# Kernel tuning notes

Measured on AMD Instinct MI355X. Metric: run time of the kernel, lower is better.

## Reference

```python
import jax, jax.numpy as jnp
import numpy as np

N = 50000   # nodes
E = 800000  # edges (avg degree 16)
D = 64      # feature dim (input_dim == hidden_dim == output_dim for num_layer=2)
BN_EPS = 1e-5


def setup_inputs() -> dict:
    key = jax.random.key(0)
    ks = jax.random.split(key, 8)
    def lin_w(k, fan_in, fan_out):
        return jax.random.normal(k, (fan_in, fan_out), jnp.float32) / np.sqrt(fan_in).astype(np.float32)
    inp = {
        "x": jax.random.normal(ks[0], (N, D), jnp.float32),
        "edge_index": jax.random.randint(ks[1], (2, E), 0, N),
    }
    ki = 2
    for l in range(2):
        for s in ("a", "b"):
            inp[f"w{l}{s}"] = lin_w(ks[ki], D, D)
            inp[f"b{l}{s}"] = jnp.zeros((D,), jnp.float32)
            inp[f"g{l}{s}"] = jnp.ones((D,), jnp.float32)   # BN gamma
            inp[f"be{l}{s}"] = jnp.zeros((D,), jnp.float32)  # BN beta
            ki += 1
    inp["lin_w"] = lin_w(ks[6], 2 * D, D)  # JK cat of 2 layers -> 2D, final lin -> D
    inp["lin_b"] = jnp.zeros((D,), jnp.float32)
    return inp


def _bn(h, g, b):
    # BatchNorm1d in training mode: batch statistics over the node axis
    m = h.mean(axis=0)
    v = h.var(axis=0)
    return (h - m) * jax.lax.rsqrt(v + BN_EPS) * g + b


def _gin(h, src, dst, w1, b1, g1, be1, w2, b2, g2, be2):
    # GINConv with eps=0: (1+eps)*x_i + sum_{j->i} x_j, then MLP(Lin-BN-ReLU-Lin-BN-ReLU)
    agg = jax.ops.segment_sum(h[src], dst, num_segments=N) + h
    h = jax.nn.relu(_bn(agg @ w1 + b1, g1, be1))
    return jax.nn.relu(_bn(h @ w2 + b2, g2, be2))


def reference(x, edge_index, w0a, b0a, g0a, be0a, w0b, b0b, g0b, be0b,
              w1a, b1a, g1a, be1a, w1b, b1b, g1b, be1b, lin_w, lin_b):
    src, dst = edge_index[0], edge_index[1]
    h1 = _gin(x, src, dst, w0a, b0a, g0a, be0a, w0b, b0b, g0b, be0b)
    h2 = _gin(h1, src, dst, w1a, b1a, g1a, be1a, w1b, b1b, g1b, be1b)
    # JumpingKnowledge 'cat' over the conv outputs (res[1:]), then final linear
    return jnp.concatenate([h1, h2], axis=1) @ lin_w + lin_b
```

## Files before the change

kernel.cpp:

```cpp
#include <hip/hip_runtime.h>
#include <hip/hip_bf16.h>

#define NN 50000
#define NE 800000
#define BN_EPS 1e-5f
#define CHUNK 8192
#define NCH 98
#define NBK 196

typedef __attribute__((ext_vector_type(4))) float f32x4;

__global__ void zero_k(int* __restrict__ p, int n) {
    int i = blockIdx.x * 256 + threadIdx.x;
    if (i < n) p[i] = 0;
}

__global__ void bhist_k(const int* __restrict__ dst, int* __restrict__ bcnt) {
    __shared__ int c[256];
    int t = threadIdx.x;
    c[t] = 0;
    __syncthreads();
    int base = blockIdx.x * CHUNK;
    int n = NE - base; if (n > CHUNK) n = CHUNK;
    for (int i = t; i < n; i += 256) atomicAdd(&c[dst[base + i] >> 8], 1);
    __syncthreads();
    if (c[t]) atomicAdd(&bcnt[t], c[t]);
}

__global__ void bscan_k(const int* __restrict__ bcnt, int* __restrict__ bbase,
                        int* __restrict__ bres, int* __restrict__ off) {
    __shared__ int s[256];
    int t = threadIdx.x;
    int v = bcnt[t];
    s[t] = v;
    __syncthreads();
    for (int d = 1; d < 256; d <<= 1) {
        int u = (t >= d) ? s[t - d] : 0;
        __syncthreads();
        s[t] += u;
        __syncthreads();
    }
    int ex = s[t] - v;
    bbase[t] = ex;
    bres[t] = ex;
    if (t == 0) { bbase[256] = NE; off[NN] = NE; }
}

__global__ void bscatter_k(const int* __restrict__ src, const int* __restrict__ dst,
                           int* __restrict__ bres, int* __restrict__ ebuf) {
    __shared__ int cnt[256], loff[256], lcur[256], gst[256], sc[256];
    __shared__ int packed[CHUNK];
    int t = threadIdx.x;
    cnt[t] = 0;
    __syncthreads();
    int base = blockIdx.x * CHUNK;
    int n = NE - base; if (n > CHUNK) n = CHUNK;
    for (int i = t; i < n; i += 256) atomicAdd(&cnt[dst[base + i] >> 8], 1);
    __syncthreads();
    sc[t] = cnt[t];
    __syncthreads();
    for (int d = 1; d < 256; d <<= 1) {
        int u = (t >= d) ? sc[t - d] : 0;
        __syncthreads();
        sc[t] += u;
        __syncthreads();
    }
    loff[t] = sc[t] - cnt[t];
    lcur[t] = loff[t];
    __syncthreads();
    for (int i = t; i < n; i += 256) {
        int d = dst[base + i];
        int b = d >> 8;
        int p = atomicAdd(&lcur[b], 1);
        packed[p] = src[base + i] | ((d & 255) << 16) | (b << 24);
    }
    __syncthreads();
    if (cnt[t]) gst[t] = atomicAdd(&bres[t], cnt[t]);
    __syncthreads();
    for (int i = t; i < n; i += 256) {
        int v = packed[i];
        int b = (v >> 24) & 255;
        ebuf[gst[b] + i - loff[b]] = v & 0xFFFFFF;
    }
}

__global__ void csr_k(const int* __restrict__ bbase, const int* __restrict__ ebuf,
                      int* __restrict__ off, int* __restrict__ adj) {
    __shared__ int cnt[256], loff[256], lcur[256], sc[256];
    int b = blockIdx.x, t = threadIdx.x;
    int s0 = bbase[b], s1 = bbase[b + 1];
    int n = s1 - s0;
    cnt[t] = 0;
    __syncthreads();
    for (int i = t; i < n; i += 256) atomicAdd(&cnt[(ebuf[s0 + i] >> 16) & 255], 1);
    __syncthreads();
    sc[t] = cnt[t];
    __syncthreads();
    for (int d = 1; d < 256; d <<= 1) {
        int u = (t >= d) ? sc[t - d] : 0;
        __syncthreads();
        sc[t] += u;
        __syncthreads();
    }
    loff[t] = sc[t] - cnt[t];
    lcur[t] = loff[t];
    int node = b * 256 + t;
    if (node < NN) off[node] = s0 + loff[t];
    __syncthreads();
    for (int i = t; i < n; i += 256) {
        int v = ebuf[s0 + i];
        int p = atomicAdd(&lcur[(v >> 16) & 255], 1);
        adj[s0 + p] = v & 0xFFFF;
    }
}

__device__ __forceinline__ float gather_row(const float* __restrict__ X, int ldx,
                                            int lane, const int* __restrict__ off,
                                            const int* __restrict__ adj, int node) {
    float acc = X[(size_t)node * ldx + lane];
    int s = off[node], e = off[node + 1];
    int p = s;
    for (; p + 8 <= e; p += 8) {
        int j0 = adj[p + 0], j1 = adj[p + 1], j2 = adj[p + 2], j3 = adj[p + 3];
        int j4 = adj[p + 4], j5 = adj[p + 5], j6 = adj[p + 6], j7 = adj[p + 7];
        float v0 = X[(size_t)j0 * ldx + lane];
        float v1 = X[(size_t)j1 * ldx + lane];
        float v2 = X[(size_t)j2 * ldx + lane];
        float v3 = X[(size_t)j3 * ldx + lane];
        float v4 = X[(size_t)j4 * ldx + lane];
        float v5 = X[(size_t)j5 * ldx + lane];
        float v6 = X[(size_t)j6 * ldx + lane];
        float v7 = X[(size_t)j7 * ldx + lane];
        acc += ((v0 + v1) + (v2 + v3)) + ((v4 + v5) + (v6 + v7));
    }
    if (p + 4 <= e) {
        int j0 = adj[p + 0], j1 = adj[p + 1], j2 = adj[p + 2], j3 = adj[p + 3];
        float v0 = X[(size_t)j0 * ldx + lane];
        float v1 = X[(size_t)j1 * ldx + lane];
        float v2 = X[(size_t)j2 * ldx + lane];
        float v3 = X[(size_t)j3 * ldx + lane];
        acc += (v0 + v1) + (v2 + v3);
        p += 4;
    }
    for (; p < e; p++) acc += X[(size_t)adj[p] * ldx + lane];
    return acc;
}

__global__ void ggemm_k(const float* __restrict__ X, int ldx,
                        const int* __restrict__ off, const int* __restrict__ adj,
                        const float* __restrict__ W,
                        const float* __restrict__ bias,
                        float* __restrict__ T,
                        float* __restrict__ sums) {
    __shared__ float As[64 * 65];
    __shared__ float Ws[64 * 64];
    __shared__ float lsum[64], lssq[64];
    int tid = threadIdx.x;
    int rowbase = blockIdx.x * 64;
    int wv = tid >> 6, lane = tid & 63;

    for (int i = tid; i < 1024; i += 256) {
        *(f32x4*)(Ws + i * 4) = *(const f32x4*)(W + i * 4);
    }
    if (tid < 64) { lsum[tid] = 0.f; lssq[tid] = 0.f; }

    for (int rr = 0; rr < 16; rr++) {
        int r = wv * 16 + rr;
        int node = rowbase + r;
        if (node >= NN) node = NN - 1;
        As[lane * 65 + r] = gather_row(X, ldx, lane, off, adj, node);
    }
    __syncthreads();

    int ty = tid >> 4, tx = tid & 15;
    float acc[4][4] = {};
    for (int k = 0; k < 64; k++) {
        float a[4], wvv[4];
        #pragma unroll
        for (int i = 0; i < 4; i++) a[i] = As[k * 65 + ty * 4 + i];
        #pragma unroll
        for (int j = 0; j < 4; j++) wvv[j] = Ws[k * 64 + tx * 4 + j];
        #pragma unroll
        for (int i = 0; i < 4; i++)
            #pragma unroll
            for (int j = 0; j < 4; j++) acc[i][j] += a[i] * wvv[j];
    }

    f32x4 bv = *(const f32x4*)(bias + tx * 4);
    float ps[4] = {0.f, 0.f, 0.f, 0.f}, pq[4] = {0.f, 0.f, 0.f, 0.f};
    #pragma unroll
    for (int i = 0; i < 4; i++) {
        int row = rowbase + ty * 4 + i;
        if (row < NN) {
            f32x4 v;
            #pragma unroll
            for (int j = 0; j < 4; j++) {
                v[j] = acc[i][j] + bv[j];
                ps[j] += v[j];
                pq[j] += v[j] * v[j];
            }
            *(f32x4*)(T + (size_t)row * 64 + tx * 4) = v;
        }
    }
    #pragma unroll
    for (int j = 0; j < 4; j++) {
        atomicAdd(&lsum[tx * 4 + j], ps[j]);
        atomicAdd(&lssq[tx * 4 + j], pq[j]);
    }
    __syncthreads();
    if (tid < 64) {
        atomicAdd(&sums[tid], lsum[tid]);
        atomicAdd(&sums[64 + tid], lssq[tid]);
    }
}

__global__ void gemm64bn_k(const float* __restrict__ Tin,
                           const float* __restrict__ stats,
                           const float* __restrict__ g,
                           const float* __restrict__ be,
                           const float* __restrict__ W,
                           const float* __restrict__ bias,
                           float* __restrict__ T,
                           float* __restrict__ sums) {
    __shared__ float As[64 * 72];
    __shared__ float Ws[64 * 64];
    __shared__ float sc[64], sh[64];
    __shared__ float lsum[64], lssq[64];
    int tid = threadIdx.x;
    int rowbase = blockIdx.x * 64;
    if (tid < 64) {
        float m = stats[tid] * (1.0f / NN);
        float var = stats[64 + tid] * (1.0f / NN) - m * m;
        if (var < 0.f) var = 0.f;
        float s = g[tid] * rsqrtf(var + BN_EPS);
        sc[tid] = s;
        sh[tid] = be[tid] - m * s;
        lsum[tid] = 0.f;
        lssq[tid] = 0.f;
    }
    __syncthreads();
    for (int i = tid; i < 64 * 16; i += 256) {
        int r = i >> 4, kq = i & 15;
        int row = rowbase + r;
        if (row >= NN) row = NN - 1;
        f32x4 v = *(const f32x4*)(Tin + (size_t)row * 64 + kq * 4);
        #pragma unroll
        for (int q = 0; q < 4; q++) {
            int k = kq * 4 + q;
            float u = v[q] * sc[k] + sh[k];
            As[k * 72 + r] = u > 0.f ? u : 0.f;
        }
    }
    for (int i = tid; i < 1024; i += 256) {
        *(f32x4*)(Ws + i * 4) = *(const f32x4*)(W + i * 4);
    }
    __syncthreads();

    int ty = tid >> 4, tx = tid & 15;
    float acc[4][4] = {};
    for (int k = 0; k < 64; k++) {
        float a[4], wv[4];
        #pragma unroll
        for (int i = 0; i < 4; i++) a[i] = As[k * 72 + ty * 4 + i];
        #pragma unroll
        for (int j = 0; j < 4; j++) wv[j] = Ws[k * 64 + tx * 4 + j];
        #pragma unroll
        for (int i = 0; i < 4; i++)
            #pragma unroll
            for (int j = 0; j < 4; j++) acc[i][j] += a[i] * wv[j];
    }

    f32x4 bv = *(const f32x4*)(bias + tx * 4);
    float ps[4] = {0.f, 0.f, 0.f, 0.f}, pq[4] = {0.f, 0.f, 0.f, 0.f};
    #pragma unroll
    for (int i = 0; i < 4; i++) {
        int row = rowbase + ty * 4 + i;
        if (row < NN) {
            f32x4 v;
            #pragma unroll
            for (int j = 0; j < 4; j++) {
                v[j] = acc[i][j] + bv[j];
                ps[j] += v[j];
                pq[j] += v[j] * v[j];
            }
            *(f32x4*)(T + (size_t)row * 64 + tx * 4) = v;
        }
    }
    #pragma unroll
    for (int j = 0; j < 4; j++) {
        atomicAdd(&lsum[tx * 4 + j], ps[j]);
        atomicAdd(&lssq[tx * 4 + j], pq[j]);
    }
    __syncthreads();
    if (tid < 64) {
        atomicAdd(&sums[tid], lsum[tid]);
        atomicAdd(&sums[64 + tid], lssq[tid]);
    }
}

__global__ void bn_k(const float* __restrict__ T, const float* __restrict__ sums,
                     const float* __restrict__ g,
                     const float* __restrict__ be,
                     float* __restrict__ H) {
    __shared__ float sc[64], sh[64];
    int tid = threadIdx.x;
    if (tid < 64) {
        float m = sums[tid] * (1.0f / NN);
        float var = sums[64 + tid] * (1.0f / NN) - m * m;
        if (var < 0.f) var = 0.f;
        float s = g[tid] * rsqrtf(var + BN_EPS);
        sc[tid] = s;
        sh[tid] = be[tid] - m * s;
    }
    __syncthreads();
    int i = blockIdx.x * 256 + tid;
    if (i < NN * 16) {
        int row = i >> 4, f = (i & 15) * 4;
        f32x4 v = *(const f32x4*)(T + (size_t)row * 64 + f);
        f32x4 u;
        #pragma unroll
        for (int j = 0; j < 4; j++) {
            float w = v[j] * sc[f + j] + sh[f + j];
            u[j] = w > 0.f ? w : 0.f;
        }
        *(f32x4*)(H + (size_t)row * 64 + f) = u;
    }
}

__global__ void gemmfin2_k(const float* __restrict__ H1,
                           const float* __restrict__ T2,
                           const float* __restrict__ stats,
                           const float* __restrict__ g,
                           const float* __restrict__ be,
                           const float* __restrict__ W,
                           const float* __restrict__ bias,
                           float* __restrict__ O) {
    __shared__ float As[128 * 72];
    __shared__ float Ws[128 * 64];
    __shared__ float sc[64], sh[64];
    int tid = threadIdx.x;
    int rowbase = blockIdx.x * 64;
    if (tid < 64) {
        float m = stats[tid] * (1.0f / NN);
        float var = stats[64 + tid] * (1.0f / NN) - m * m;
        if (var < 0.f) var = 0.f;
        float s = g[tid] * rsqrtf(var + BN_EPS);
        sc[tid] = s;
        sh[tid] = be[tid] - m * s;
    }
    __syncthreads();
    for (int i = tid; i < 64 * 16; i += 256) {
        int r = i >> 4, kq = i & 15;
        int row = rowbase + r;
        if (row >= NN) row = NN - 1;
        f32x4 v1 = *(const f32x4*)(H1 + (size_t)row * 64 + kq * 4);
        f32x4 v2 = *(const f32x4*)(T2 + (size_t)row * 64 + kq * 4);
        #pragma unroll
        for (int q = 0; q < 4; q++) {
            int k = kq * 4 + q;
            As[k * 72 + r] = v1[q];
            float u = v2[q] * sc[k] + sh[k];
            As[(64 + k) * 72 + r] = u > 0.f ? u : 0.f;
        }
    }
    for (int i = tid; i < 2048; i += 256) {
        *(f32x4*)(Ws + i * 4) = *(const f32x4*)(W + i * 4);
    }
    __syncthreads();

    int ty = tid >> 4, tx = tid & 15;
    float acc[4][4] = {};
    for (int k = 0; k < 128; k++) {
        float a[4], wv[4];
        #pragma unroll
        for (int i = 0; i < 4; i++) a[i] = As[k * 72 + ty * 4 + i];
        #pragma unroll
        for (int j = 0; j < 4; j++) wv[j] = Ws[k * 64 + tx * 4 + j];
        #pragma unroll
        for (int i = 0; i < 4; i++)
            #pragma unroll
            for (int j = 0; j < 4; j++) acc[i][j] += a[i] * wv[j];
    }

    f32x4 bv = *(const f32x4*)(bias + tx * 4);
    #pragma unroll
    for (int i = 0; i < 4; i++) {
        int row = rowbase + ty * 4 + i;
        if (row < NN) {
            f32x4 v;
            #pragma unroll
            for (int j = 0; j < 4; j++) v[j] = acc[i][j] + bv[j];
            *(f32x4*)(O + (size_t)row * 64 + tx * 4) = v;
        }
    }
}

extern "C" void kernel_launch(void* const* d_in, const int* in_sizes, int n_in,
                              void* d_out, int out_size, void* d_ws, size_t ws_size,
                              hipStream_t stream) {
    const float* x   = (const float*)d_in[0];
    const int*   ei  = (const int*)d_in[1];
    const float* w0a = (const float*)d_in[2];
    const float* b0a = (const float*)d_in[3];
    const float* g0a = (const float*)d_in[4];
    const float* be0a= (const float*)d_in[5];
    const float* w0b = (const float*)d_in[6];
    const float* b0b = (const float*)d_in[7];
    const float* g0b = (const float*)d_in[8];
    const float* be0b= (const float*)d_in[9];
    const float* w1a = (const float*)d_in[10];
    const float* b1a = (const float*)d_in[11];
    const float* g1a = (const float*)d_in[12];
    const float* be1a= (const float*)d_in[13];
    const float* w1b = (const float*)d_in[14];
    const float* b1b = (const float*)d_in[15];
    const float* g1b = (const float*)d_in[16];
    const float* be1b= (const float*)d_in[17];
    const float* lw  = (const float*)d_in[18];
    const float* lb  = (const float*)d_in[19];
    float* out = (float*)d_out;
    (void)in_sizes; (void)n_in; (void)out_size; (void)ws_size;

    char* wsb = (char*)d_ws;
    size_t o = 0;
    auto alloc = [&](size_t bytes) -> char* {
        char* p = wsb + o;
        o += (bytes + 255) & ~(size_t)255;
        return p;
    };
    int* bcnt = (int*)alloc(256 * 4);
    float* sums = (float*)alloc(512 * 4);
    int* bbase = (int*)alloc(257 * 4);
    int* bres = (int*)alloc(256 * 4);
    int* off = (int*)alloc((NN + 1) * 4);
    int* adj = (int*)alloc(NE * 4);
    int* ebuf = (int*)alloc(NE * 4);
    float* T   = (float*)alloc((size_t)NN * 64 * 4);
    float* T2  = (float*)alloc((size_t)NN * 64 * 4);
    float* HC  = (float*)alloc((size_t)NN * 64 * 4);

    const int* src = ei;
    const int* dst = ei + NE;

    zero_k<<<3, 256, 0, stream>>>((int*)d_ws, 768);
    bhist_k<<<NCH, 256, 0, stream>>>(dst, bcnt);
    bscan_k<<<1, 256, 0, stream>>>(bcnt, bbase, bres, off);
    bscatter_k<<<NCH, 256, 0, stream>>>(src, dst, bres, ebuf);
    csr_k<<<NBK, 256, 0, stream>>>(bbase, ebuf, off, adj);

    const int mgrid = (NN + 63) / 64;
    const int agrid = (NN * 16 + 255) / 256;

    ggemm_k<<<mgrid, 256, 0, stream>>>(x, 64, off, adj, w0a, b0a, T, sums + 0);
    gemm64bn_k<<<mgrid, 256, 0, stream>>>(T, sums + 0, g0a, be0a, w0b, b0b, T2, sums + 128);
    bn_k<<<agrid, 256, 0, stream>>>(T2, sums + 128, g0b, be0b, HC);

    ggemm_k<<<mgrid, 256, 0, stream>>>(HC, 64, off, adj, w1a, b1a, T, sums + 256);
    gemm64bn_k<<<mgrid, 256, 0, stream>>>(T, sums + 256, g1a, be1a, w1b, b1b, T2, sums + 384);

    gemmfin2_k<<<mgrid, 256, 0, stream>>>(HC, T2, sums + 384, g1b, be1b, lw, lb, out);
}
```

Measured before the change: 380.0 us.

## Gather neighbors from bf16 feature copies in a separate kernel before GEMM

After: 355.2 us. -6.5%, faster.

```diff
diff --git a/kernel.cpp b/kernel.cpp
--- a/kernel.cpp
+++ b/kernel.cpp
@@ -9,10 +9,27 @@
 #define NBK 196
 
 typedef __attribute__((ext_vector_type(4))) float f32x4;
+typedef __attribute__((ext_vector_type(4))) short s16x4;
+
+__device__ __forceinline__ float bf2f(__hip_bfloat16 v) { return __bfloat162float(v); }
 
 __global__ void zero_k(int* __restrict__ p, int n) {
     int i = blockIdx.x * 256 + threadIdx.x;
     if (i < n) p[i] = 0;
+}
+
+__global__ void cvt_k(const float* __restrict__ X, __hip_bfloat16* __restrict__ Xb) {
+    int i = blockIdx.x * 256 + threadIdx.x;
+    if (i < NN * 16) {
+        f32x4 v = *(const f32x4*)(X + (size_t)i * 4);
+        s16x4 ov;
+        #pragma unroll
+        for (int j = 0; j < 4; j++) {
+            __hip_bfloat16 b = __float2bfloat16(v[j]);
+            ov[j] = __builtin_bit_cast(short, b);
+        }
+        *(s16x4*)((short*)Xb + (size_t)i * 4) = ov;
+    }
 }
 
 __global__ void bhist_k(const int* __restrict__ dst, int* __restrict__ bcnt) {
@@ -114,76 +131,77 @@
     }
 }
 
-__device__ __forceinline__ float gather_row(const float* __restrict__ X, int ldx,
-                                            int lane, const int* __restrict__ off,
-                                            const int* __restrict__ adj, int node) {
-    float acc = X[(size_t)node * ldx + lane];
+__global__ void gather_k(const __hip_bfloat16* __restrict__ X,
+                         const int* __restrict__ off, const int* __restrict__ adj,
+                         float* __restrict__ AGG) {
+    int node = blockIdx.x * 4 + (threadIdx.x >> 6);
+    int lane = threadIdx.x & 63;
+    if (node >= NN) return;
+    float acc = bf2f(X[(size_t)node * 64 + lane]);
     int s = off[node], e = off[node + 1];
     int p = s;
     for (; p + 8 <= e; p += 8) {
         int j0 = adj[p + 0], j1 = adj[p + 1], j2 = adj[p + 2], j3 = adj[p + 3];
         int j4 = adj[p + 4], j5 = adj[p + 5], j6 = adj[p + 6], j7 = adj[p + 7];
-        float v0 = X[(size_t)j0 * ldx + lane];
-        float v1 = X[(size_t)j1 * ldx + lane];
-        float v2 = X[(size_t)j2 * ldx + lane];
-        float v3 = X[(size_t)j3 * ldx + lane];
-        float v4 = X[(size_t)j4 * ldx + lane];
-        float v5 = X[(size_t)j5 * ldx + lane];
-        float v6 = X[(size_t)j6 * ldx + lane];
-        float v7 = X[(size_t)j7 * ldx + lane];
+        float v0 = bf2f(X[(size_t)j0 * 64 + lane]);
+        float v1 = bf2f(X[(size_t)j1 * 64 + lane]);
+        float v2 = bf2f(X[(size_t)j2 * 64 + lane]);
+        float v3 = bf2f(X[(size_t)j3 * 64 + lane]);
+        float v4 = bf2f(X[(size_t)j4 * 64 + lane]);
+        float v5 = bf2f(X[(size_t)j5 * 64 + lane]);
+        float v6 = bf2f(X[(size_t)j6 * 64 + lane]);
+        float v7 = bf2f(X[(size_t)j7 * 64 + lane]);
         acc += ((v0 + v1) + (v2 + v3)) + ((v4 + v5) + (v6 + v7));
     }
     if (p + 4 <= e) {
         int j0 = adj[p + 0], j1 = adj[p + 1], j2 = adj[p + 2], j3 = adj[p + 3];
-        float v0 = X[(size_t)j0 * ldx + lane];
-        float v1 = X[(size_t)j1 * ldx + lane];
-        float v2 = X[(size_t)j2 * ldx + lane];
-        float v3 = X[(size_t)j3 * ldx + lane];
+        float v0 = bf2f(X[(size_t)j0 * 64 + lane]);
+        float v1 = bf2f(X[(size_t)j1 * 64 + lane]);
+        float v2 = bf2f(X[(size_t)j2 * 64 + lane]);
+        float v3 = bf2f(X[(size_t)j3 * 64 + lane]);
         acc += (v0 + v1) + (v2 + v3);
         p += 4;
     }
-    for (; p < e; p++) acc += X[(size_t)adj[p] * ldx + lane];
-    return acc;
-}
-
-__global__ void ggemm_k(const float* __restrict__ X, int ldx,
-                        const int* __restrict__ off, const int* __restrict__ adj,
-                        const float* __restrict__ W,
-                        const float* __restrict__ bias,
-                        float* __restrict__ T,
-                        float* __restrict__ sums) {
-    __shared__ float As[64 * 65];
+    for (; p < e; p++) acc += bf2f(X[(size_t)adj[p] * 64 + lane]);
+    AGG[(size_t)node * 64 + lane] = acc;
+}
+
+__global__ void gemm64_k(const float* __restrict__ A,
+                         const float* __restrict__ W,
+                         const float* __restrict__ bias,
+                         float* __restrict__ T,
+                         float* __restrict__ sums) {
+    __shared__ float As[64 * 72];
     __shared__ float Ws[64 * 64];
     __shared__ float lsum[64], lssq[64];
     int tid = threadIdx.x;
     int rowbase = blockIdx.x * 64;
-    int wv = tid >> 6, lane = tid & 63;
-
+    for (int i = tid; i < 64 * 16; i += 256) {
+        int r = i >> 4, kq = i & 15;
+        int row = rowbase + r;
+        if (row >= NN) row = NN - 1;
+        f32x4 v = *(const f32x4*)(A + (size_t)row * 64 + kq * 4);
+        #pragma unroll
+        for (int q = 0; q < 4; q++) As[(kq * 4 + q) * 72 + r] = v[q];
+    }
     for (int i = tid; i < 1024; i += 256) {
         *(f32x4*)(Ws + i * 4) = *(const f32x4*)(W + i * 4);
     }
     if (tid < 64) { lsum[tid] = 0.f; lssq[tid] = 0.f; }
-
-    for (int rr = 0; rr < 16; rr++) {
-        int r = wv * 16 + rr;
-        int node = rowbase + r;
-        if (node >= NN) node = NN - 1;
-        As[lane * 65 + r] = gather_row(X, ldx, lane, off, adj, node);
-    }
     __syncthreads();
 
     int ty = tid >> 4, tx = tid & 15;
     float acc[4][4] = {};
     for (int k = 0; k < 64; k++) {
-        float a[4], wvv[4];
-        #pragma unroll
-        for (int i = 0; i < 4; i++) a[i] = As[k * 65 + ty * 4 + i];
-        #pragma unroll
-        for (int j = 0; j < 4; j++) wvv[j] = Ws[k * 64 + tx * 4 + j];
+        float a[4], wv[4];
+        #pragma unroll
+        for (int i = 0; i < 4; i++) a[i] = As[k * 72 + ty * 4 + i];
+        #pragma unroll
+        for (int j = 0; j < 4; j++) wv[j] = Ws[k * 64 + tx * 4 + j];
         #pragma unroll
         for (int i = 0; i < 4; i++)
             #pragma unroll
-            for (int j = 0; j < 4; j++) acc[i][j] += a[i] * wvv[j];
+            for (int j = 0; j < 4; j++) acc[i][j] += a[i] * wv[j];
     }
 
     f32x4 bv = *(const f32x4*)(bias + tx * 4);
@@ -301,7 +319,7 @@
 __global__ void bn_k(const float* __restrict__ T, const float* __restrict__ sums,
                      const float* __restrict__ g,
                      const float* __restrict__ be,
-                     float* __restrict__ H) {
+                     float* __restrict__ H, __hip_bfloat16* __restrict__ Hb) {
     __shared__ float sc[64], sh[64];
     int tid = threadIdx.x;
     if (tid < 64) {
@@ -318,12 +336,16 @@
         int row = i >> 4, f = (i & 15) * 4;
         f32x4 v = *(const f32x4*)(T + (size_t)row * 64 + f);
         f32x4 u;
+        s16x4 ub;
         #pragma unroll
         for (int j = 0; j < 4; j++) {
             float w = v[j] * sc[f + j] + sh[f + j];
             u[j] = w > 0.f ? w : 0.f;
+            __hip_bfloat16 b = __float2bfloat16(u[j]);
+            ub[j] = __builtin_bit_cast(short, b);
         }
         *(f32x4*)(H + (size_t)row * 64 + f) = u;
+        *(s16x4*)((short*)Hb + (size_t)row * 64 + f) = ub;
     }
 }
 
@@ -435,9 +457,12 @@
     int* off = (int*)alloc((NN + 1) * 4);
     int* adj = (int*)alloc(NE * 4);
     int* ebuf = (int*)alloc(NE * 4);
+    float* AGG = (float*)alloc((size_t)NN * 64 * 4);
     float* T   = (float*)alloc((size_t)NN * 64 * 4);
     float* T2  = (float*)alloc((size_t)NN * 64 * 4);
     float* HC  = (float*)alloc((size_t)NN * 64 * 4);
+    __hip_bfloat16* Xb  = (__hip_bfloat16*)alloc((size_t)NN * 64 * 2);
+    __hip_bfloat16* HCb = (__hip_bfloat16*)alloc((size_t)NN * 64 * 2);
 
     const int* src = ei;
     const int* dst = ei + NE;
@@ -448,14 +473,19 @@
     bscatter_k<<<NCH, 256, 0, stream>>>(src, dst, bres, ebuf);
     csr_k<<<NBK, 256, 0, stream>>>(bbase, ebuf, off, adj);
 
+    const int ggrid = NN / 4;
     const int mgrid = (NN + 63) / 64;
     const int agrid = (NN * 16 + 255) / 256;
 
-    ggemm_k<<<mgrid, 256, 0, stream>>>(x, 64, off, adj, w0a, b0a, T, sums + 0);
+    cvt_k<<<agrid, 256, 0, stream>>>(x, Xb);
+
+    gather_k<<<ggrid, 256, 0, stream>>>(Xb, off, adj, AGG);
+    gemm64_k<<<mgrid, 256, 0, stream>>>(AGG, w0a, b0a, T, sums + 0);
     gemm64bn_k<<<mgrid, 256, 0, stream>>>(T, sums + 0, g0a, be0a, w0b, b0b, T2, sums + 128);
-    bn_k<<<agrid, 256, 0, stream>>>(T2, sums + 128, g0b, be0b, HC);
-
-    ggemm_k<<<mgrid, 256, 0, stream>>>(HC, 64, off, adj, w1a, b1a, T, sums + 256);
+    bn_k<<<agrid, 256, 0, stream>>>(T2, sums + 128, g0b, be0b, HC, HCb);
+
+    gather_k<<<ggrid, 256, 0, stream>>>(HCb, off, adj, AGG);
+    gemm64_k<<<mgrid, 256, 0, stream>>>(AGG, w1a, b1a, T, sums + 256);
     gemm64bn_k<<<mgrid, 256, 0, stream>>>(T, sums + 256, g1a, be1a, w1b, b1b, T2, sums + 384);
 
     gemmfin2_k<<<mgrid, 256, 0, stream>>>(HC, T2, sums + 384, g1b, be1b, lw, lb, out);
```
